# Optimization experiments

Measured on AMD Instinct MI355X. Metric: run time of the kernel, lower is better.

Reference implementation:

```python
import jax, jax.numpy as jnp
import numpy as np

H = 128      # hidden_channels
G = 512      # number of graphs in the batch
NEG_SLOPE = 0.2


def _seg_sum(x, idx, n):
    return jax.ops.segment_sum(x, idx, num_segments=n)


def _sage(x_src, x_dst, ei, Wl, bl, Wr):
    # PyG SAGEConv: lin_l(mean_j x_j) + lin_r(x_i); lin_l has bias, lin_r does not.
    s, d = ei[0], ei[1]
    n = x_dst.shape[0]
    agg = _seg_sum(x_src[s], d, n)
    cnt = _seg_sum(jnp.ones((ei.shape[1],), x_src.dtype), d, n)
    mean = agg / jnp.maximum(cnt, 1.0)[:, None]
    return mean @ Wl + bl + x_dst @ Wr


def _gat(x_src, x_dst, ei, Ws, Wd, a_s, a_d, b):
    # PyG GATConv (heads=1, add_self_loops=False, bipartite): segment softmax over dst.
    s, d = ei[0], ei[1]
    n = x_dst.shape[0]
    hs = x_src @ Ws                                  # [N_src, H]
    hd = x_dst @ Wd                                  # [N_dst, H]
    logit = jax.nn.leaky_relu((hs @ a_s)[s] + (hd @ a_d)[d], NEG_SLOPE)
    m = jax.ops.segment_max(logit, d, num_segments=n)
    e = jnp.exp(logit - m[d])
    z = _seg_sum(e, d, n)
    alpha = e / jnp.maximum(z[d], 1e-16)
    return _seg_sum(alpha[:, None] * hs[s], d, n) + b


def _gcn(x, ei, W, b):
    # PyG GCNConv with add_self_loops=True, normalize=True (same src/dst node type).
    s, d = ei[0], ei[1]
    n = x.shape[0]
    deg = _seg_sum(jnp.ones((ei.shape[1],), x.dtype), d, n) + 1.0  # +1 self loop
    dis = jax.lax.rsqrt(deg)
    h = x @ W
    norm = dis[s] * dis[d]
    out = _seg_sum(norm[:, None] * h[s], d, n) + (dis * dis)[:, None] * h
    return out + b


def _pool(x, b):
    s = _seg_sum(x, b, G)
    c = _seg_sum(jnp.ones((x.shape[0],), x.dtype), b, G)
    return s / jnp.maximum(c, 1.0)[:, None]


def setup_inputs() -> dict:
    key = jax.random.key(0)
    ks = iter(jax.random.split(key, 80))
    scale = 1.0 / np.sqrt(H)

    def nrm(shape, sc=scale):
        return jax.random.normal(next(ks), shape, jnp.float32) * sc

    def edges(e, n_src, n_dst):
        src = jax.random.randint(next(ks), (e,), 0, n_src, jnp.int32)
        dst = jax.random.randint(next(ks), (e,), 0, n_dst, jnp.int32)
        return jnp.stack([src, dst])

    def batch(n):
        return jnp.sort(jax.random.randint(next(ks), (n,), 0, G, jnp.int32))

    N_CD, N_SEQ, N_ANNO, N_RANGE, N_MD = 100000, 80000, 80000, 80000, 50000
    inp = {
        'x_cd': nrm((N_CD, H), 1.0), 'x_seq': nrm((N_SEQ, H), 1.0),
        'x_anno': nrm((N_ANNO, H), 1.0), 'x_range': nrm((N_RANGE, H), 1.0),
        'x_md': nrm((N_MD, H), 1.0),
        'ei_seq': edges(160000, N_CD, N_SEQ),
        'ei_anno': edges(200000, N_CD, N_ANNO),
        'ei_range': edges(200000, N_CD, N_RANGE),
        'ei_comp': edges(300000, N_MD, N_CD),
        'ei_cc': edges(300000, N_CD, N_CD),
        'ei_mm': edges(150000, N_MD, N_MD),
        'b_cd': batch(N_CD), 'b_seq': batch(N_SEQ), 'b_anno': batch(N_ANNO),
        'b_range': batch(N_RANGE), 'b_md': batch(N_MD),
    }
    # per-layer stacked params (leading axis = 2 layers)
    for nm, shp in [('Wsl_seq', (2, H, H)), ('bs_seq', (2, H)), ('Wsr_seq', (2, H, H)),
                    ('Wsl_anno', (2, H, H)), ('bs_anno', (2, H)), ('Wsr_anno', (2, H, H)),
                    ('Wg_comp_s', (2, H, H)), ('Wg_comp_d', (2, H, H)),
                    ('ag_comp_s', (2, H)), ('ag_comp_d', (2, H)), ('bg_comp', (2, H)),
                    ('Wg_range_s', (2, H, H)), ('Wg_range_d', (2, H, H)),
                    ('ag_range_s', (2, H)), ('ag_range_d', (2, H)), ('bg_range', (2, H)),
                    ('Wc_cc', (2, H, H)), ('bc_cc', (2, H)),
                    ('Wc_mm', (2, H, H)), ('bc_mm', (2, H)),
                    ('lin1_W', (5 * H, H)), ('lin1_b', (H,)),
                    ('lin2_W', (H, 1)), ('lin2_b', (1,))]:
        inp[nm] = nrm(shp)
    return inp


def reference(x_cd, x_seq, x_anno, x_range, x_md,
              ei_seq, ei_anno, ei_range, ei_comp, ei_cc, ei_mm,
              b_cd, b_seq, b_anno, b_range, b_md,
              Wsl_seq, bs_seq, Wsr_seq, Wsl_anno, bs_anno, Wsr_anno,
              Wg_comp_s, Wg_comp_d, ag_comp_s, ag_comp_d, bg_comp,
              Wg_range_s, Wg_range_d, ag_range_s, ag_range_d, bg_range,
              Wc_cc, bc_cc, Wc_mm, bc_mm,
              lin1_W, lin1_b, lin2_W, lin2_b):
    for l in range(2):
        # HeteroConv aggr='sum': CD receives GAT(MD->CD) + GCN(CD->CD)
        n_cd = (_gat(x_md, x_cd, ei_comp, Wg_comp_s[l], Wg_comp_d[l],
                     ag_comp_s[l], ag_comp_d[l], bg_comp[l])
                + _gcn(x_cd, ei_cc, Wc_cc[l], bc_cc[l]))
        n_seq = _sage(x_cd, x_seq, ei_seq, Wsl_seq[l], bs_seq[l], Wsr_seq[l])
        n_anno = _sage(x_cd, x_anno, ei_anno, Wsl_anno[l], bs_anno[l], Wsr_anno[l])
        n_range = _gat(x_cd, x_range, ei_range, Wg_range_s[l], Wg_range_d[l],
                       ag_range_s[l], ag_range_d[l], bg_range[l])
        n_md = _gcn(x_md, ei_mm, Wc_mm[l], bc_mm[l])
        x_cd, x_seq, x_anno, x_range, x_md = (
            jax.nn.relu(n_cd), jax.nn.relu(n_seq), jax.nn.relu(n_anno),
            jax.nn.relu(n_range), jax.nn.relu(n_md))
    emb = jnp.concatenate([_pool(x_cd, b_cd), _pool(x_seq, b_seq),
                           _pool(x_anno, b_anno), _pool(x_range, b_range),
                           _pool(x_md, b_md)], axis=-1)        # [G, 5H]
    h = jax.nn.relu(emb @ lin1_W + lin1_b)  # Dropout(0.7) is identity in eval
    return (h @ lin2_W + lin2_b).reshape(-1)  # [G]
```

## Files before the change

### kernel.cpp

```cpp
#include <hip/hip_runtime.h>

#define HD 128
#define GNUM 512
#define RPB 520
#define IDXCAP 512
#define TM 32

typedef __attribute__((ext_vector_type(8))) short short8v;
typedef __attribute__((ext_vector_type(4))) float f32x4;

__device__ __forceinline__ void split1(float a, short& h, short& l) {
  unsigned u = __float_as_uint(a);
  unsigned hb = (u + 0x7FFFu + ((u >> 16) & 1u)) & 0xFFFF0000u;
  h = (short)(hb >> 16);
  float rest = a - __uint_as_float(hb);
  unsigned u2 = __float_as_uint(rest);
  l = (short)((u2 + 0x7FFFu + ((u2 >> 16) & 1u)) >> 16);
}

struct WTab { const float* p[8]; };
__global__ __launch_bounds__(256) void k_split_w(WTab tab, short* __restrict__ whi,
                                                 short* __restrict__ wlo)
{
  int m = blockIdx.x >> 6;
  int i = (blockIdx.x & 63) * 256 + threadIdx.x;
  const float* W = tab.p[m >> 1] + (m & 1) * 16384;
  int k = i >> 7, n = i & 127;
  short h, l;
  split1(W[k * 128 + n], h, l);
  whi[m * 16384 + n * 128 + k] = h;
  wlo[m * 16384 + n * 128 + k] = l;
}

struct COp {
  const float* A; const short* WH; const short* WL;
  const int* grp; const int* gcol;
  const float* wsrc; const float* rowsc; int mode;
};
#define CF_LD 132
__global__ __launch_bounds__(256) void k_gemm_conv(
    COp o0, COp o1, int hasO1,
    float* __restrict__ C, const float* __restrict__ bias, const float* __restrict__ bias2,
    const float* addin, int N, int relu,
    const float* __restrict__ avec, float* __restrict__ adot,
    const float* __restrict__ avec2, float* __restrict__ adot2)
{
  __shared__ char smem[TM * 136 * 2 * 2];
  __shared__ int idxbuf[IDXCAP];
  __shared__ float wbuf[IDXCAP];
  short* Ah = (short*)smem;
  short* Al = Ah + TM * 136;
  float* Cf = (float*)smem;

  const int t = threadIdx.x;
  const int row0 = blockIdx.x * TM;
  const int lane = t & 63, wid = t >> 6;
  const int g = lane >> 4, cn = lane & 15;
  const int colbase = wid * 32;

  f32x4 zero = {0.f, 0.f, 0.f, 0.f};
  f32x4 acc[2][2];
#pragma unroll
  for (int rt = 0; rt < 2; ++rt) { acc[rt][0] = zero; acc[rt][1] = zero; }

  auto storeAhl = [&](int row, int ln, float4 s) {
    short4 h, l;
    split1(s.x, h.x, l.x); split1(s.y, h.y, l.y);
    split1(s.z, h.z, l.z); split1(s.w, h.w, l.w);
    *(short4*)(Ah + row * 136 + ln * 4) = h;
    *(short4*)(Al + row * 136 + ln * 4) = l;
  };

  auto stageA = [&](const float* __restrict__ A) {
#pragma unroll
    for (int i = 0; i < 4; ++i) {
      int f4 = t + i * 256;
      int row = f4 >> 5, c4 = f4 & 31;
      float4 v = make_float4(0.f, 0.f, 0.f, 0.f);
      if (row0 + row < N) v = ((const float4*)(A + (size_t)row0 * 128))[f4];
      storeAhl(row, c4, v);
    }
  };

  auto prefetch = [&](const COp& op) {
    const int row_end = min(row0 + TM, N);
    const int e_lo = op.grp[row0];
    const int cnt = min(op.grp[row_end] - e_lo, IDXCAP);
    for (int k = t; k < cnt; k += 256) {
      int idx = op.gcol[e_lo + k];
      idxbuf[k] = idx;
      if (op.wsrc) wbuf[k] = op.wsrc[idx];
    }
  };

  auto stage_gather = [&](const COp& op) {
    const int e_lo = op.grp[row0];
    const int mode = op.mode;
    const float* X = op.A;
    auto getcw = [&](int e, int& c, float& w) {
      int off = e - e_lo;
      if (off < IDXCAP) { c = idxbuf[off]; w = wbuf[off]; }
      else { c = op.gcol[e]; w = op.wsrc ? op.wsrc[c] : 0.f; }
    };
#pragma unroll
    for (int i = 0; i < 4; ++i) {
      int f4 = t + i * 256;
      int row = f4 >> 5, ln = f4 & 31;
      int r = row0 + row;
      float4 s = make_float4(0.f, 0.f, 0.f, 0.f);
      int e0 = 0, e1 = 0;
      float rs = 0.f;
      if (r < N) {
        e0 = op.grp[r]; e1 = op.grp[r + 1];
        if (mode >= 2) rs = op.rowsc[r];
      }
      float z = 0.f;
      if (mode == 2 && r < N) {
        float4 xs_ = *(const float4*)(X + (size_t)r * 128 + ln * 4);
        float rr = rs * rs;
        s.x = rr * xs_.x; s.y = rr * xs_.y; s.z = rr * xs_.z; s.w = rr * xs_.w;
      }
      int e = e0;
      for (; e + 1 < e1; e += 2) {
        int c0, c1; float w0, w1;
        getcw(e, c0, w0);
        getcw(e + 1, c1, w1);
        float p0, p1;
        if (mode == 3) {
          float v0 = w0 + rs; v0 = v0 > 0.f ? v0 : 0.2f * v0;
          float v1 = w1 + rs; v1 = v1 > 0.f ? v1 : 0.2f * v1;
          p0 = __expf(v0); p1 = __expf(v1); z += p0 + p1;
        } else if (mode == 2) { p0 = w0 * rs; p1 = w1 * rs; }
        else { p0 = 1.f; p1 = 1.f; }
        float4 a = *(const float4*)(X + (size_t)c0 * 128 + ln * 4);
        float4 b = *(const float4*)(X + (size_t)c1 * 128 + ln * 4);
        s.x += p0 * a.x + p1 * b.x; s.y += p0 * a.y + p1 * b.y;
        s.z += p0 * a.z + p1 * b.z; s.w += p0 * a.w + p1 * b.w;
      }
      if (e < e1) {
        int c; float w;
        getcw(e, c, w);
        float p;
        if (mode == 3) {
          float v = w + rs; v = v > 0.f ? v : 0.2f * v;
          p = __expf(v); z += p;
        } else if (mode == 2) p = w * rs;
        else p = 1.f;
        float4 a = *(const float4*)(X + (size_t)c * 128 + ln * 4);
        s.x += p * a.x; s.y += p * a.y; s.z += p * a.z; s.w += p * a.w;
      }
      if (mode == 1) {
        float inv = 1.f / fmaxf((float)(e1 - e0), 1.f);
        s.x *= inv; s.y *= inv; s.z *= inv; s.w *= inv;
      } else if (mode == 3) {
        float inv = (e1 > e0) ? 1.f / z : 0.f;
        s.x *= inv; s.y *= inv; s.z *= inv; s.w *= inv;
      }
      storeAhl(row, ln, s);
    }
  };

  auto accum = [&](const short* __restrict__ WH, const short* __restrict__ WL) {
#pragma unroll
    for (int kg = 0; kg < 4; ++kg) {
      short8v bhi[2], blo[2];
#pragma unroll
      for (int ct = 0; ct < 2; ++ct) {
        size_t o = (size_t)(colbase + ct * 16 + cn) * 128 + kg * 32 + g * 8;
        bhi[ct] = *(const short8v*)(WH + o);
        blo[ct] = *(const short8v*)(WL + o);
      }
#pragma unroll
      for (int rt = 0; rt < 2; ++rt) {
        const int ao = (rt * 16 + cn) * 136 + kg * 32 + g * 8;
        const short8v ah = *(const short8v*)(Ah + ao);
        const short8v al = *(const short8v*)(Al + ao);
#pragma unroll
        for (int ct = 0; ct < 2; ++ct) {
          acc[rt][ct] = __builtin_amdgcn_mfma_f32_16x16x32_bf16(ah, bhi[ct], acc[rt][ct], 0, 0, 0);
          acc[rt][ct] = __builtin_amdgcn_mfma_f32_16x16x32_bf16(al, bhi[ct], acc[rt][ct], 0, 0, 0);
          acc[rt][ct] = __builtin_amdgcn_mfma_f32_16x16x32_bf16(ah, blo[ct], acc[rt][ct], 0, 0, 0);
        }
      }
    }
  };

  if (o0.mode) {
    prefetch(o0);
    __syncthreads();
    stage_gather(o0);
  } else {
    stageA(o0.A);
  }
  __syncthreads();
  if (hasO1 && o1.mode) prefetch(o1);
  accum(o0.WH, o0.WL);
  if (hasO1) {
    __syncthreads();
    if (o1.mode) stage_gather(o1); else stageA(o1.A);
    __syncthreads();
    accum(o1.WH, o1.WL);
  }
  __syncthreads();

#pragma unroll
  for (int rt = 0; rt < 2; ++rt)
#pragma unroll
    for (int ct = 0; ct < 2; ++ct)
#pragma unroll
      for (int r = 0; r < 4; ++r)
        Cf[(rt * 16 + g * 4 + r) * CF_LD + colbase + ct * 16 + cn] = acc[rt][ct][r];
  __syncthreads();

  float4* C4 = (float4*)(C + (size_t)row0 * 128);
#pragma unroll
  for (int i = 0; i < 4; ++i) {
    int f4 = t + i * 256;
    int row = f4 >> 5, c4 = f4 & 31;
    if (row0 + row < N) {
      float4 v = *(const float4*)(Cf + row * CF_LD + c4 * 4);
      if (bias) {
        float4 bv = *(const float4*)(bias + c4 * 4);
        v.x += bv.x; v.y += bv.y; v.z += bv.z; v.w += bv.w;
      }
      if (bias2) {
        float4 bv = *(const float4*)(bias2 + c4 * 4);
        v.x += bv.x; v.y += bv.y; v.z += bv.z; v.w += bv.w;
      }
      if (addin) {
        float4 av = *(const float4*)(addin + (size_t)(row0 + row) * 128 + c4 * 4);
        v.x += av.x; v.y += av.y; v.z += av.z; v.w += av.w;
      }
      if (relu) {
        v.x = fmaxf(v.x, 0.f); v.y = fmaxf(v.y, 0.f);
        v.z = fmaxf(v.z, 0.f); v.w = fmaxf(v.w, 0.f);
      }
      C4[f4] = v;
      if (avec) {
        float4 av = *(const float4*)(avec + c4 * 4);
        float p = v.x * av.x + v.y * av.y + v.z * av.z + v.w * av.w;
#pragma unroll
        for (int o = 1; o < 32; o <<= 1) p += __shfl_xor(p, o);
        if (c4 == 0) adot[row0 + row] = p;
      }
      if (avec2) {
        float4 av = *(const float4*)(avec2 + c4 * 4);
        float p = v.x * av.x + v.y * av.y + v.z * av.z + v.w * av.w;
#pragma unroll
        for (int o = 1; o < 32; o <<= 1) p += __shfl_xor(p, o);
        if (c4 == 0) adot2[row0 + row] = p;
      }
    }
  }
}

__global__ void k_rowdot(const float* __restrict__ x, const float* __restrict__ a,
                         float* __restrict__ out, int N)
{
  int wid = blockIdx.x * 4 + (threadIdx.x >> 6);
  int lane = threadIdx.x & 63;
  if (wid >= N) return;
  float2 xv = ((const float2*)x)[(size_t)wid * 64 + lane];
  float2 av = ((const float2*)a)[lane];
  float v = fmaf(xv.y, av.y, xv.x * av.x);
#pragma unroll
  for (int o = 32; o > 0; o >>= 1) v += __shfl_down(v, o);
  if (lane == 0) out[wid] = v;
}

__global__ void k_rowdot2(const float* __restrict__ x, const float* __restrict__ a1,
                          const float* __restrict__ a2, float* __restrict__ o1,
                          float* __restrict__ o2, int N)
{
  int wid = blockIdx.x * 4 + (threadIdx.x >> 6);
  int lane = threadIdx.x & 63;
  if (wid >= N) return;
  float2 xv = ((const float2*)x)[(size_t)wid * 64 + lane];
  float2 av1 = ((const float2*)a1)[lane];
  float2 av2 = ((const float2*)a2)[lane];
  float v1 = fmaf(xv.y, av1.y, xv.x * av1.x);
  float v2 = fmaf(xv.y, av2.y, xv.x * av2.x);
#pragma unroll
  for (int o = 32; o > 0; o >>= 1) { v1 += __shfl_down(v1, o); v2 += __shfl_down(v2, o); }
  if (lane == 0) { o1[wid] = v1; o2[wid] = v2; }
}

struct MTab { const float* W[8]; const float* a[8]; };
__global__ __launch_bounds__(128) void k_matvec8(MTab tb, float* __restrict__ wv)
{
  __shared__ float as[128];
  int m = blockIdx.x, i = threadIdx.x;
  as[i] = tb.a[m][i];
  __syncthreads();
  const float* W = tb.W[m];
  float v = 0.f;
  for (int j = 0; j < 128; ++j) v = fmaf(W[i * 128 + j], as[j], v);
  wv[m * 128 + i] = v;
}

struct HTab { const int* key[6]; int* cnt[6]; unsigned short* rank[6]; int bo[7]; int n[6]; };
__global__ void k_hist_rank_all(HTab tb) {
  int bi = blockIdx.x, ty = 0;
  while (ty < 5 && bi >= tb.bo[ty + 1]) ++ty;
  int i = (bi - tb.bo[ty]) * 256 + threadIdx.x;
  if (i < tb.n[ty])
    tb.rank[ty][i] = (unsigned short)atomicAdd(&tb.cnt[ty][tb.key[ty][i]], 1);
}

struct FTab { const int* es[6]; const int* ed[6]; const int* rp[6];
              const unsigned short* rank[6]; int* col[6]; int bo[7]; int n[6]; };
__global__ void k_fill_all(FTab tb) {
  int bi = blockIdx.x, ty = 0;
  while (ty < 5 && bi >= tb.bo[ty + 1]) ++ty;
  int e = (bi - tb.bo[ty]) * 256 + threadIdx.x;
  if (e >= tb.n[ty]) return;
  int p = tb.rp[ty][tb.ed[ty][e]] + (int)tb.rank[ty][e];
  tb.col[ty][p] = tb.es[ty][e];
}

struct STab { int* rp[6]; int* bs[6]; int n[6]; int bo[7]; };

__global__ __launch_bounds__(256) void k_scan_partial_all(STab tb) {
  __shared__ int red[256];
  int bi = blockIdx.x, ty = 0;
  while (ty < 5 && bi >= tb.bo[ty + 1]) ++ty;
  int lb = bi - tb.bo[ty];
  const int* rp = tb.rp[ty];
  const int N = tb.n[ty];
  const int t = threadIdx.x, base = lb * 4096;
  int s = 0;
  for (int i = t; i < 4096; i += 256) {
    int idx = base + i;
    if (idx < N) s += rp[idx];
  }
  red[t] = s;
  __syncthreads();
  for (int ofs = 128; ofs > 0; ofs >>= 1) {
    if (t < ofs) red[t] += red[t + ofs];
    __syncthreads();
  }
  if (t == 0) tb.bs[ty][lb] = red[0];
}

__global__ __launch_bounds__(256) void k_scan_bsums_all(STab tb) {
  __shared__ int sh[256];
  const int ty = blockIdx.x;
  const int nb = (tb.n[ty] + 4095) / 4096;
  const int t = threadIdx.x;
  int v = (t < nb) ? tb.bs[ty][t] : 0;
  sh[t] = v;
  __syncthreads();
  for (int ofs = 1; ofs < 256; ofs <<= 1) {
    int u = (t >= ofs) ? sh[t - ofs] : 0;
    __syncthreads();
    sh[t] += u;
    __syncthreads();
  }
  if (t < nb) tb.bs[ty][t] = sh[t] - v;
  if (t == 255) tb.rp[ty][tb.n[ty]] = sh[255];
}

__global__ __launch_bounds__(256) void k_scan_final_all(STab tb) {
  __shared__ int sh[4096 + 256];
  __shared__ int tsum[256];
  int bi = blockIdx.x, ty = 0;
  while (ty < 5 && bi >= tb.bo[ty + 1]) ++ty;
  int lb = bi - tb.bo[ty];
  int* rp = tb.rp[ty];
  const int N = tb.n[ty];
  const int t = threadIdx.x, base = lb * 4096;
  auto mp = [](int i) { return i + (i >> 4); };
#pragma unroll
  for (int i = 0; i < 16; ++i) {
    int idx = base + i * 256 + t;
    sh[mp(i * 256 + t)] = (idx < N) ? rp[idx] : 0;
  }
  __syncthreads();
  int s = 0;
#pragma unroll
  for (int j = 0; j < 16; ++j) s += sh[mp(t * 16 + j)];
  tsum[t] = s;
  __syncthreads();
  for (int ofs = 1; ofs < 256; ofs <<= 1) {
    int u = (t >= ofs) ? tsum[t - ofs] : 0;
    __syncthreads();
    tsum[t] += u;
    __syncthreads();
  }
  int pre = tsum[t] - s + tb.bs[ty][lb];
#pragma unroll
  for (int j = 0; j < 16; ++j) {
    int v = sh[mp(t * 16 + j)];
    sh[mp(t * 16 + j)] = pre;
    pre += v;
  }
  __syncthreads();
#pragma unroll
  for (int i = 0; i < 16; ++i) {
    int idx = base + i * 256 + t;
    if (idx < N) rp[idx] = sh[mp(i * 256 + t)];
  }
}

struct BTab { const int* b[5]; int n[5]; };
__global__ __launch_bounds__(512) void k_runptr(BTab tb, int* __restrict__ rpb_all) {
  const int ty = blockIdx.x;
  const int* b = tb.b[ty];
  const int N = tb.n[ty];
  const int t = threadIdx.x;
  int lo = 0, hi = N;
  while (lo < hi) {
    int mid = (lo + hi) >> 1;
    if (b[mid] < t) lo = mid + 1; else hi = mid;
  }
  rpb_all[ty * RPB + t] = lo;
  if (t == 0) rpb_all[ty * RPB + GNUM] = N;
}

struct DTab { const int* rp[2]; float* dis[2]; int n[2]; int bo[3]; };
__global__ void k_dis2(DTab tb) {
  int bi = blockIdx.x, ty = (bi >= tb.bo[1]) ? 1 : 0;
  int n = (bi - tb.bo[ty]) * 256 + threadIdx.x;
  if (n < tb.n[ty]) tb.dis[ty][n] = rsqrtf((float)(tb.rp[ty][n + 1] - tb.rp[ty][n]) + 1.f);
}

__global__ __launch_bounds__(256) void k_pool_seg(
    const float* __restrict__ x, const int* __restrict__ rpb,
    float* __restrict__ pool, int col_off)
{
  __shared__ float2 red2[4][64];
  const int g = blockIdx.x;
  const int t = threadIdx.x, w = t >> 6, lane = t & 63;
  const int n0 = rpb[g], n1 = rpb[g + 1];
  const float2* x2 = (const float2*)x;
  float a0 = 0.f, a1 = 0.f, b0 = 0.f, b1 = 0.f;
  int n = n0 + w;
  for (; n + 4 < n1; n += 8) {
    float2 vA = x2[(size_t)n * 64 + lane];
    float2 vB = x2[(size_t)(n + 4) * 64 + lane];
    a0 += vA.x; a1 += vA.y; b0 += vB.x; b1 += vB.y;
  }
  if (n < n1) { float2 vA = x2[(size_t)n * 64 + lane]; a0 += vA.x; a1 += vA.y; }
  red2[w][lane] = make_float2(a0 + b0, a1 + b1);
  __syncthreads();
  if (t < 64) {
    float2 r0 = red2[0][t], r1 = red2[1][t], r2 = red2[2][t], r3 = red2[3][t];
    float inv = 1.f / fmaxf((float)(n1 - n0), 1.f);
    ((float2*)(pool + (size_t)g * 640 + col_off))[t] =
        make_float2((r0.x + r1.x + r2.x + r3.x) * inv,
                    (r0.y + r1.y + r2.y + r3.y) * inv);
  }
}

__global__ void k_mlp(const float* __restrict__ pool,
                      const float* __restrict__ W1, const float* __restrict__ b1,
                      const float* __restrict__ W2, const float* __restrict__ b2,
                      float* __restrict__ out)
{
  __shared__ float emb[640];
  __shared__ float red[128];
  const int g = blockIdx.x, t = threadIdx.x;
  for (int i = t; i < 640; i += 128) emb[i] = pool[(size_t)g * 640 + i];
  __syncthreads();
  float acc = b1[t];
  for (int i = 0; i < 640; ++i) acc = fmaf(emb[i], W1[i * 128 + t], acc);
  float h = fmaxf(acc, 0.f);
  red[t] = h * W2[t];
  __syncthreads();
  for (int s = 64; s > 0; s >>= 1) {
    if (t < s) red[t] += red[t + s];
    __syncthreads();
  }
  if (t == 0) out[g] = red[0] + b2[0];
}

extern "C" void kernel_launch(void* const* d_in, const int* in_sizes, int n_in,
                              void* d_out, int out_size, void* d_ws, size_t ws_size,
                              hipStream_t stream)
{
  auto fin = [&](int i) { return (const float*)d_in[i]; };
  auto iin = [&](int i) { return (const int*)d_in[i]; };

  const float *x_cd = fin(0), *x_seq = fin(1), *x_anno = fin(2), *x_range = fin(3), *x_md = fin(4);
  const int *ei_seq = iin(5), *ei_anno = iin(6), *ei_range = iin(7),
            *ei_comp = iin(8), *ei_cc = iin(9), *ei_mm = iin(10);
  const int *b_cd = iin(11), *b_seq = iin(12), *b_anno = iin(13), *b_range = iin(14), *b_md = iin(15);

  const int N_CD = in_sizes[0] / HD, N_SEQ = in_sizes[1] / HD, N_ANNO = in_sizes[2] / HD,
            N_RANGE = in_sizes[3] / HD, N_MD = in_sizes[4] / HD;
  const int E_seq = in_sizes[5] / 2, E_anno = in_sizes[6] / 2, E_range = in_sizes[7] / 2,
            E_comp = in_sizes[8] / 2, E_cc = in_sizes[9] / 2, E_mm = in_sizes[10] / 2;
  const int N_OTH = max(max(N_SEQ, N_ANNO), N_RANGE);

  auto WLm = [&](int i, int l) { return fin(i) + (size_t)l * HD * HD; };
  auto WLv = [&](int i, int l) { return fin(i) + (size_t)l * HD; };

  float* ws = (float*)d_ws;
  size_t off = 0;
  auto alloc = [&](size_t n) { float* p = ws + off; off += (n + 3) & ~(size_t)3; return p; };
  float* xcd1 = alloc((size_t)N_CD * HD);
  float* xmd1 = alloc((size_t)N_MD * HD);
  float* xoth = alloc((size_t)N_OTH * HD);
  float* acc  = alloc((size_t)N_CD * HD);
  float* t1   = alloc((size_t)N_CD * HD);
  float* sA = alloc((size_t)N_CD);
  float* sB = alloc((size_t)N_CD);
  float* sC = alloc((size_t)N_CD);
  float* sD = alloc((size_t)N_CD);
  float* sE = alloc((size_t)N_CD);
  float* sF = alloc((size_t)N_CD);
  float* dis_cc = alloc((size_t)N_CD);
  float* dis_mm = alloc((size_t)N_MD);
  float* wv8 = alloc(8 * HD);
  float* pool = alloc((size_t)GNUM * 5 * HD);
  short* whi = (short*)(ws + off); off += (size_t)16 * 16384 / 2;
  short* wlo = (short*)(ws + off); off += (size_t)16 * 16384 / 2;
  auto alloci = [&](size_t n) { int* p = (int*)(ws + off); off += (n + 3) & ~(size_t)3; return p; };
  int* bsall = alloci(6 * 256);
  int* rpb_all = alloci(5 * RPB);
  int Nds[6] = {N_SEQ, N_ANNO, N_RANGE, N_CD, N_CD, N_MD};
  int Es[6]  = {E_seq, E_anno, E_range, E_comp, E_cc, E_mm};
  int* rps[6];
  int* rp0 = alloci(0);
  { size_t tot = 0; for (int i = 0; i < 6; ++i) tot += (size_t)Nds[i] + 1;
    int* p = alloci(tot); rp0 = p;
    for (int i = 0; i < 6; ++i) { rps[i] = p; p += Nds[i] + 1; } }
  size_t rp_tot_bytes = 0; for (int i = 0; i < 6; ++i) rp_tot_bytes += ((size_t)Nds[i] + 1) * 4;
  unsigned short* ranks[6];
  for (int i = 0; i < 6; ++i) ranks[i] = (unsigned short*)alloci(((size_t)Es[i] + 1) / 2);
  int* cols[6];  for (int i = 0; i < 6; ++i) cols[i] = alloci((size_t)Es[i]);
  (void)n_in;

  if (off * sizeof(float) > ws_size) {
    hipMemsetAsync(d_out, 0, (size_t)out_size * sizeof(float), stream);
    return;
  }

  auto ew = [&](size_t elems) { return dim3((unsigned)((elems + 255) / 256)); };
  auto nw = [&](int N) { return dim3((unsigned)((N + 3) / 4)); };

  WTab tab;
  tab.p[0] = fin(16); tab.p[1] = fin(18); tab.p[2] = fin(19); tab.p[3] = fin(21);
  tab.p[4] = fin(22); tab.p[5] = fin(27); tab.p[6] = fin(32); tab.p[7] = fin(34);
  k_split_w<<<dim3(1024), dim3(256), 0, stream>>>(tab, whi, wlo);

  MTab mt;
  mt.W[0] = WLm(22, 0); mt.a[0] = WLv(24, 0);
  mt.W[1] = WLm(23, 0); mt.a[1] = WLv(25, 0);
  mt.W[2] = WLm(22, 1); mt.a[2] = WLv(24, 1);
  mt.W[3] = WLm(23, 1); mt.a[3] = WLv(25, 1);
  mt.W[4] = WLm(27, 0); mt.a[4] = WLv(29, 0);
  mt.W[5] = WLm(28, 0); mt.a[5] = WLv(30, 0);
  mt.W[6] = WLm(27, 1); mt.a[6] = WLv(29, 1);
  mt.W[7] = WLm(28, 1); mt.a[7] = WLv(30, 1);
  k_matvec8<<<dim3(8), dim3(128), 0, stream>>>(mt, wv8);

  k_rowdot<<<nw(N_MD), dim3(256), 0, stream>>>(x_md, wv8 + 0 * 128, sA, N_MD);
  k_rowdot2<<<nw(N_CD), dim3(256), 0, stream>>>(x_cd, wv8 + 1 * 128, wv8 + 4 * 128,
                                                sB, sC, N_CD);
  k_rowdot<<<nw(N_RANGE), dim3(256), 0, stream>>>(x_range, wv8 + 5 * 128, sD, N_RANGE);

  {
    BTab bt;
    bt.b[0] = b_cd; bt.n[0] = N_CD;  bt.b[1] = b_seq; bt.n[1] = N_SEQ;
    bt.b[2] = b_anno; bt.n[2] = N_ANNO;  bt.b[3] = b_range; bt.n[3] = N_RANGE;
    bt.b[4] = b_md; bt.n[4] = N_MD;
    k_runptr<<<dim3(5), dim3(512), 0, stream>>>(bt, rpb_all);
  }

  const int* ess[6] = {ei_seq, ei_anno, ei_range, ei_comp, ei_cc, ei_mm};
  const int* eds[6] = {ei_seq + E_seq, ei_anno + E_anno, ei_range + E_range,
                       ei_comp + E_comp, ei_cc + E_cc, ei_mm + E_mm};
  hipMemsetAsync(rp0, 0, rp_tot_bytes, stream);
  {
    HTab ht; int b = 0;
    for (int i = 0; i < 6; ++i) {
      ht.key[i] = eds[i]; ht.cnt[i] = rps[i]; ht.rank[i] = ranks[i];
      ht.bo[i] = b; b += (Es[i] + 255) / 256; ht.n[i] = Es[i];
    }
    ht.bo[6] = b;
    k_hist_rank_all<<<dim3(b), dim3(256), 0, stream>>>(ht);
  }
  {
    STab st; int b = 0;
    for (int i = 0; i < 6; ++i) {
      st.rp[i] = rps[i]; st.bs[i] = bsall + i * 256;
      st.n[i] = Nds[i]; st.bo[i] = b; b += (Nds[i] + 4095) / 4096;
    }
    st.bo[6] = b;
    k_scan_partial_all<<<dim3(b), dim3(256), 0, stream>>>(st);
    k_scan_bsums_all<<<dim3(6), dim3(256), 0, stream>>>(st);
    k_scan_final_all<<<dim3(b), dim3(256), 0, stream>>>(st);
  }
  {
    FTab ft; int b = 0;
    for (int i = 0; i < 6; ++i) {
      ft.es[i] = ess[i]; ft.ed[i] = eds[i]; ft.rp[i] = rps[i]; ft.rank[i] = ranks[i];
      ft.col[i] = cols[i]; ft.bo[i] = b; b += (Es[i] + 255) / 256; ft.n[i] = Es[i];
    }
    ft.bo[6] = b;
    k_fill_all<<<dim3(b), dim3(256), 0, stream>>>(ft);
  }
  int *rp_seq = rps[0], *rp_anno = rps[1], *rp_range = rps[2],
      *rp_comp = rps[3], *rp_cc = rps[4], *rp_mm = rps[5];
  int *col_seq = cols[0], *col_anno = cols[1], *col_range = cols[2],
      *col_comp = cols[3], *col_cc = cols[4], *col_mm = cols[5];
  {
    DTab dt;
    dt.rp[0] = rp_cc; dt.dis[0] = dis_cc; dt.n[0] = N_CD;
    dt.rp[1] = rp_mm; dt.dis[1] = dis_mm; dt.n[1] = N_MD;
    dt.bo[0] = 0; dt.bo[1] = (N_CD + 255) / 256;
    dt.bo[2] = dt.bo[1] + (N_MD + 255) / 256;
    k_dis2<<<dim3(dt.bo[2]), dim3(256), 0, stream>>>(dt);
  }

  auto WHp = [&](int sidx, int layer) { return whi + (size_t)(sidx * 2 + layer) * 16384; };
  auto WLp = [&](int sidx, int layer) { return wlo + (size_t)(sidx * 2 + layer) * 16384; };

  auto mkop = [&](int mode, const float* A, int sidx, int layer,
                  const int* grp, const int* gcol,
                  const float* wsrc, const float* rowsc) {
    COp o;
    o.A = A; o.WH = WHp(sidx, layer); o.WL = WLp(sidx, layer);
    o.grp = grp; o.gcol = gcol; o.wsrc = wsrc; o.rowsc = rowsc; o.mode = mode;
    return o;
  };
  auto launch = [&](COp o0, COp o1, int hasO1, float* C, const float* bias,
                    const float* bias2, const float* addin, int N, int relu,
                    const float* avec, float* adot, const float* avec2, float* adot2) {
    k_gemm_conv<<<dim3((N + TM - 1) / TM), dim3(256), 0, stream>>>(
        o0, o1, hasO1, C, bias, bias2, addin, N, relu, avec, adot, avec2, adot2);
  };
  auto do_pool = [&](const float* x, int type) {
    k_pool_seg<<<dim3(GNUM), dim3(256), 0, stream>>>(x, rpb_all + type * RPB, pool, type * HD);
  };
  COp nop = {};

  launch(mkop(3, x_md, 4, 0, rp_comp, col_comp, sA, sB),
         mkop(2, x_cd, 6, 0, rp_cc, col_cc, dis_cc, dis_cc), 1,
         xcd1, WLv(26, 0), WLv(33, 0), nullptr, N_CD, 1,
         wv8 + 3 * 128, sB, wv8 + 6 * 128, sE);
  launch(mkop(2, x_md, 7, 0, rp_mm, col_mm, dis_mm, dis_mm), nop, 0,
         xmd1, WLv(35, 0), nullptr, nullptr, N_MD, 1,
         wv8 + 2 * 128, sA, nullptr, nullptr);
  launch(mkop(3, xmd1, 4, 1, rp_comp, col_comp, sA, sB),
         mkop(2, xcd1, 6, 1, rp_cc, col_cc, dis_cc, dis_cc), 1,
         acc, WLv(26, 1), WLv(33, 1), nullptr, N_CD, 1,
         nullptr, nullptr, nullptr, nullptr);
  do_pool(acc, 0);
  launch(mkop(2, xmd1, 7, 1, rp_mm, col_mm, dis_mm, dis_mm), nop, 0,
         acc, WLv(35, 1), nullptr, nullptr, N_MD, 1,
         nullptr, nullptr, nullptr, nullptr);
  do_pool(acc, 4);

  launch(mkop(1, x_cd, 0, 0, rp_seq, col_seq, nullptr, nullptr),
         mkop(0, x_seq, 1, 0, nullptr, nullptr, nullptr, nullptr), 1,
         xoth, WLv(17, 0), nullptr, nullptr, N_SEQ, 1, nullptr, nullptr, nullptr, nullptr);
  launch(mkop(1, xcd1, 0, 1, rp_seq, col_seq, nullptr, nullptr),
         mkop(0, xoth, 1, 1, nullptr, nullptr, nullptr, nullptr), 1,
         acc, WLv(17, 1), nullptr, nullptr, N_SEQ, 1, nullptr, nullptr, nullptr, nullptr);
  do_pool(acc, 1);
  launch(mkop(1, x_cd, 2, 0, rp_anno, col_anno, nullptr, nullptr),
         mkop(0, x_anno, 3, 0, nullptr, nullptr, nullptr, nullptr), 1,
         t1, WLv(20, 0), nullptr, nullptr, N_ANNO, 1, nullptr, nullptr, nullptr, nullptr);
  launch(mkop(1, xcd1, 2, 1, rp_anno, col_anno, nullptr, nullptr),
         mkop(0, t1, 3, 1, nullptr, nullptr, nullptr, nullptr), 1,
         acc, WLv(20, 1), nullptr, nullptr, N_ANNO, 1, nullptr, nullptr, nullptr, nullptr);
  do_pool(acc, 2);
  launch(mkop(3, x_cd, 5, 0, rp_range, col_range, sC, sD), nop, 0,
         xoth, WLv(31, 0), nullptr, nullptr, N_RANGE, 1,
         wv8 + 7 * 128, sF, nullptr, nullptr);
  launch(mkop(3, xcd1, 5, 1, rp_range, col_range, sE, sF), nop, 0,
         acc, WLv(31, 1), nullptr, nullptr, N_RANGE, 1,
         nullptr, nullptr, nullptr, nullptr);
  do_pool(acc, 3);

  k_mlp<<<dim3(GNUM), dim3(128), 0, stream>>>(
      pool, fin(36), fin(37), fin(38), fin(39), (float*)d_out);
}
```

Measured before the change: 884.4 us.

## Fuse mean-pooling into final-layer GEMM epilogue via atomic segment sums

```diff
diff --git a/kernel.cpp b/kernel.cpp
--- a/kernel.cpp
+++ b/kernel.cpp
@@ -43,11 +43,13 @@
     float* __restrict__ C, const float* __restrict__ bias, const float* __restrict__ bias2,
     const float* addin, int N, int relu,
     const float* __restrict__ avec, float* __restrict__ adot,
-    const float* __restrict__ avec2, float* __restrict__ adot2)
+    const float* __restrict__ avec2, float* __restrict__ adot2,
+    const int* __restrict__ bvec, float* __restrict__ poolbuf, int coloff)
 {
   __shared__ char smem[TM * 136 * 2 * 2];
   __shared__ int idxbuf[IDXCAP];
   __shared__ float wbuf[IDXCAP];
+  __shared__ int bsh[TM];
   short* Ah = (short*)smem;
   short* Al = Ah + TM * 136;
   float* Cf = (float*)smem;
@@ -212,7 +214,7 @@
         Cf[(rt * 16 + g * 4 + r) * CF_LD + colbase + ct * 16 + cn] = acc[rt][ct][r];
   __syncthreads();
 
-  float4* C4 = (float4*)(C + (size_t)row0 * 128);
+  float4* C4 = C ? (float4*)(C + (size_t)row0 * 128) : nullptr;
 #pragma unroll
   for (int i = 0; i < 4; ++i) {
     int f4 = t + i * 256;
@@ -235,7 +237,8 @@
         v.x = fmaxf(v.x, 0.f); v.y = fmaxf(v.y, 0.f);
         v.z = fmaxf(v.z, 0.f); v.w = fmaxf(v.w, 0.f);
       }
-      C4[f4] = v;
+      if (C) C4[f4] = v;
+      *(float4*)(Cf + row * CF_LD + c4 * 4) = v;
       if (avec) {
         float4 av = *(const float4*)(avec + c4 * 4);
         float p = v.x * av.x + v.y * av.y + v.z * av.z + v.w * av.w;
@@ -250,6 +253,26 @@
         for (int o = 1; o < 32; o <<= 1) p += __shfl_xor(p, o);
         if (c4 == 0) adot2[row0 + row] = p;
       }
+    }
+  }
+
+  if (poolbuf) {
+    if (t < TM) { int r = row0 + t; bsh[t] = (r < N) ? bvec[r] : -1; }
+    __syncthreads();
+    if (t < 128) {
+      int c = t;
+      float sum = 0.f;
+      int cur = bsh[0];
+      for (int r = 0; r < TM; ++r) {
+        int gg = bsh[r];
+        if (gg < 0) break;
+        if (gg != cur) {
+          atomicAdd(poolbuf + (size_t)cur * 640 + coloff + c, sum);
+          sum = 0.f; cur = gg;
+        }
+        sum += Cf[r * CF_LD + c];
+      }
+      if (cur >= 0) atomicAdd(poolbuf + (size_t)cur * 640 + coloff + c, sum);
     }
   }
 }
@@ -424,35 +447,7 @@
   if (n < tb.n[ty]) tb.dis[ty][n] = rsqrtf((float)(tb.rp[ty][n + 1] - tb.rp[ty][n]) + 1.f);
 }
 
-__global__ __launch_bounds__(256) void k_pool_seg(
-    const float* __restrict__ x, const int* __restrict__ rpb,
-    float* __restrict__ pool, int col_off)
-{
-  __shared__ float2 red2[4][64];
-  const int g = blockIdx.x;
-  const int t = threadIdx.x, w = t >> 6, lane = t & 63;
-  const int n0 = rpb[g], n1 = rpb[g + 1];
-  const float2* x2 = (const float2*)x;
-  float a0 = 0.f, a1 = 0.f, b0 = 0.f, b1 = 0.f;
-  int n = n0 + w;
-  for (; n + 4 < n1; n += 8) {
-    float2 vA = x2[(size_t)n * 64 + lane];
-    float2 vB = x2[(size_t)(n + 4) * 64 + lane];
-    a0 += vA.x; a1 += vA.y; b0 += vB.x; b1 += vB.y;
-  }
-  if (n < n1) { float2 vA = x2[(size_t)n * 64 + lane]; a0 += vA.x; a1 += vA.y; }
-  red2[w][lane] = make_float2(a0 + b0, a1 + b1);
-  __syncthreads();
-  if (t < 64) {
-    float2 r0 = red2[0][t], r1 = red2[1][t], r2 = red2[2][t], r3 = red2[3][t];
-    float inv = 1.f / fmaxf((float)(n1 - n0), 1.f);
-    ((float2*)(pool + (size_t)g * 640 + col_off))[t] =
-        make_float2((r0.x + r1.x + r2.x + r3.x) * inv,
-                    (r0.y + r1.y + r2.y + r3.y) * inv);
-  }
-}
-
-__global__ void k_mlp(const float* __restrict__ pool,
+__global__ void k_mlp(const float* __restrict__ pool, const int* __restrict__ rpb_all,
                       const float* __restrict__ W1, const float* __restrict__ b1,
                       const float* __restrict__ W2, const float* __restrict__ b2,
                       float* __restrict__ out)
@@ -460,7 +455,11 @@
   __shared__ float emb[640];
   __shared__ float red[128];
   const int g = blockIdx.x, t = threadIdx.x;
-  for (int i = t; i < 640; i += 128) emb[i] = pool[(size_t)g * 640 + i];
+  for (int i = t; i < 640; i += 128) {
+    int type = i >> 7;
+    int cnt = rpb_all[type * RPB + g + 1] - rpb_all[type * RPB + g];
+    emb[i] = pool[(size_t)g * 640 + i] / fmaxf((float)cnt, 1.f);
+  }
   __syncthreads();
   float acc = b1[t];
   for (int i = 0; i < 640; ++i) acc = fmaf(emb[i], W1[i * 128 + t], acc);
@@ -501,7 +500,6 @@
   float* xcd1 = alloc((size_t)N_CD * HD);
   float* xmd1 = alloc((size_t)N_MD * HD);
   float* xoth = alloc((size_t)N_OTH * HD);
-  float* acc  = alloc((size_t)N_CD * HD);
   float* t1   = alloc((size_t)N_CD * HD);
   float* sA = alloc((size_t)N_CD);
   float* sB = alloc((size_t)N_CD);
@@ -539,6 +537,8 @@
   auto ew = [&](size_t elems) { return dim3((unsigned)((elems + 255) / 256)); };
   auto nw = [&](int N) { return dim3((unsigned)((N + 3) / 4)); };
 
+  hipMemsetAsync(pool, 0, (size_t)GNUM * 5 * HD * sizeof(float), stream);
+
   WTab tab;
   tab.p[0] = fin(16); tab.p[1] = fin(18); tab.p[2] = fin(19); tab.p[3] = fin(21);
   tab.p[4] = fin(22); tab.p[5] = fin(27); tab.p[6] = fin(32); tab.p[7] = fin(34);
@@ -627,54 +627,52 @@
   };
   auto launch = [&](COp o0, COp o1, int hasO1, float* C, const float* bias,
                     const float* bias2, const float* addin, int N, int relu,
-                    const float* avec, float* adot, const float* avec2, float* adot2) {
+                    const float* avec, float* adot, const float* avec2, float* adot2,
+                    const int* bvec, int coloff) {
     k_gemm_conv<<<dim3((N + TM - 1) / TM), dim3(256), 0, stream>>>(
-        o0, o1, hasO1, C, bias, bias2, addin, N, relu, avec, adot, avec2, adot2);
-  };
-  auto do_pool = [&](const float* x, int type) {
-    k_pool_seg<<<dim3(GNUM), dim3(256), 0, stream>>>(x, rpb_all + type * RPB, pool, type * HD);
+        o0, o1, hasO1, C, bias, bias2, addin, N, relu, avec, adot, avec2, adot2,
+        bvec, bvec ? pool : nullptr, coloff);
   };
   COp nop = {};
 
   launch(mkop(3, x_md, 4, 0, rp_comp, col_comp, sA, sB),
          mkop(2, x_cd, 6, 0, rp_cc, col_cc, dis_cc, dis_cc), 1,
          xcd1, WLv(26, 0), WLv(33, 0), nullptr, N_CD, 1,
-         wv8 + 3 * 128, sB, wv8 + 6 * 128, sE);
+         wv8 + 3 * 128, sB, wv8 + 6 * 128, sE, nullptr, 0);
   launch(mkop(2, x_md, 7, 0, rp_mm, col_mm, dis_mm, dis_mm), nop, 0,
          xmd1, WLv(35, 0), nullptr, nullptr, N_MD, 1,
-         wv8 + 2 * 128, sA, nullptr, nullptr);
+         wv8 + 2 * 128, sA, nullptr, nullptr, nullptr, 0);
   launch(mkop(3, xmd1, 4, 1, rp_comp, col_comp, sA, sB),
          mkop(2, xcd1, 6, 1, rp_cc, col_cc, dis_cc, dis_cc), 1,
-         acc, WLv(26, 1), WLv(33, 1), nullptr, N_CD, 1,
-         nullptr, nullptr, nullptr, nullptr);
-  do_pool(acc, 0);
+         nullptr, WLv(26, 1), WLv(33, 1), nullptr, N_CD, 1,
+         nullptr, nullptr, nullptr, nullptr, b_cd, 0 * HD);
   launch(mkop(2, xmd1, 7, 1, rp_mm, col_mm, dis_mm, dis_mm), nop, 0,
-         acc, WLv(35, 1), nullptr, nullptr, N_MD, 1,
-         nullptr, nullptr, nullptr, nullptr);
-  do_pool(acc, 4);
+         nullptr, WLv(35, 1), nullptr, nullptr, N_MD, 1,
+         nullptr, nullptr, nullptr, nullptr, b_md, 4 * HD);
 
   launch(mkop(1, x_cd, 0, 0, rp_seq, col_seq, nullptr, nullptr),
          mkop(0, x_seq, 1, 0, nullptr, nullptr, nullptr, nullptr), 1,
-         xoth, WLv(17, 0), nullptr, nullptr, N_SEQ, 1, nullptr, nullptr, nullptr, nullptr);
+         xoth, WLv(17, 0), nullptr, nullptr, N_SEQ, 1,
+         nullptr, nullptr, nullptr, nullptr, nullptr, 0);
   launch(mkop(1, xcd1, 0, 1, rp_seq, col_seq, nullptr, nullptr),
          mkop(0, xoth, 1, 1, nullptr, nullptr, nullptr, nullptr), 1,
-         acc, WLv(17, 1), nullptr, nullptr, N_SEQ, 1, nullptr, nullptr, nullptr, nullptr);
-  do_pool(acc, 1);
+         nullptr, WLv(17, 1), nullptr, nullptr, N_SEQ, 1,
+         nullptr, nullptr, nullptr, nullptr, b_seq, 1 * HD);
   launch(mkop(1, x_cd, 2, 0, rp_anno, col_anno, nullptr, nullptr),
          mkop(0, x_anno, 3, 0, nullptr, nullptr, nullptr, nullptr), 1,
-         t1, WLv(20, 0), nullptr, nullptr, N_ANNO, 1, nullptr, nullptr, nullptr, nullptr);
+         t1, WLv(20, 0), nullptr, nullptr, N_ANNO, 1,
+         nullptr, nullptr, nullptr, nullptr, nullptr, 0);
   launch(mkop(1, xcd1, 2, 1, rp_anno, col_anno, nullptr, nullptr),
          mkop(0, t1, 3, 1, nullptr, nullptr, nullptr, nullptr), 1,
-         acc, WLv(20, 1), nullptr, nullptr, N_ANNO, 1, nullptr, nullptr, nullptr, nullptr);
-  do_pool(acc, 2);
+         nullptr, WLv(20, 1), nullptr, nullptr, N_ANNO, 1,
+         nullptr, nullptr, nullptr, nullptr, b_anno, 2 * HD);
   launch(mkop(3, x_cd, 5, 0, rp_range, col_range, sC, sD), nop, 0,
          xoth, WLv(31, 0), nullptr, nullptr, N_RANGE, 1,
-         wv8 + 7 * 128, sF, nullptr, nullptr);
+         wv8 + 7 * 128, sF, nullptr, nullptr, nullptr, 0);
   launch(mkop(3, xcd1, 5, 1, rp_range, col_range, sE, sF), nop, 0,
-         acc, WLv(31, 1), nullptr, nullptr, N_RANGE, 1,
-         nullptr, nullptr, nullptr, nullptr);
-  do_pool(acc, 3);
+         nullptr, WLv(31, 1), nullptr, nullptr, N_RANGE, 1,
+         nullptr, nullptr, nullptr, nullptr, b_range, 3 * HD);
 
   k_mlp<<<dim3(GNUM), dim3(128), 0, stream>>>(
-      pool, fin(36), fin(37), fin(38), fin(39), (float*)d_out);
-}
+      pool, rpb_all, fin(36), fin(37), fin(38), fin(39), (float*)d_out);
+}
```

Result: faster. 844.7 us (-4.5%).
